# Optimization experiments

Measured on AMD Instinct MI355X. Metric: run time of the kernel, lower is better.

## Reference

```python
import jax, jax.numpy as jnp
import numpy as np

N = 8192          # num nodes
D = 512           # num_hidden
P = 512           # num_proj_hidden
TAU = 0.5
EPS = 1e-12       # F.normalize eps


def setup_inputs() -> dict:
    key = jax.random.key(0)
    k1, k2, k3, k4, k5, k6 = jax.random.split(key, 6)
    s1 = 1.0 / np.sqrt(D)  # torch Linear init bound
    s2 = 1.0 / np.sqrt(P)
    return {
        "z1": jax.random.normal(k1, (N, D), jnp.float32),
        "z2": jax.random.normal(k2, (N, D), jnp.float32),
        "index": jnp.arange(N, dtype=jnp.int32),  # all-unique -> unique() identity path
        "fc1_w": jax.random.uniform(k3, (D, P), jnp.float32, -s1, s1),
        "fc1_b": jax.random.uniform(k4, (P,), jnp.float32, -s1, s1),
        "fc2_w": jax.random.uniform(k5, (P, D), jnp.float32, -s2, s2),
        "fc2_b": jax.random.uniform(k6, (D,), jnp.float32, -s2, s2),
    }


def _projection(z, fc1_w, fc1_b, fc2_w, fc2_b):
    h = jax.nn.elu(z @ fc1_w + fc1_b)
    return h @ fc2_w + fc2_b


def _normalize(x):
    n = jnp.linalg.norm(x, axis=1, keepdims=True)
    return x / jnp.maximum(n, EPS)


def _semi_loss(a, b):
    an = _normalize(a)
    bn = _normalize(b)
    refl = jnp.exp((an @ an.T) / TAU)      # [N, N]
    btw = jnp.exp((an @ bn.T) / TAU)       # [N, N]
    denom = refl.sum(axis=1) + btw.sum(axis=1) - jnp.diagonal(refl)
    return -jnp.log(jnp.diagonal(btw) / denom)  # [N]


def reference(z1, z2, index, fc1_w, fc1_b, fc2_w, fc2_b):
    h1 = _projection(z1, fc1_w, fc1_b, fc2_w, fc2_b)
    h2 = _projection(z2, fc1_w, fc1_b, fc2_w, fc2_b)
    # index is all-unique (arange) -> unique() returns (h1, h2) unchanged
    l1 = _semi_loss(h1, h2)
    l2 = _semi_loss(h2, h1)
    return ((l1 + l2) * 0.5).mean()
```

## Files before the change

### kernel.cpp

```cpp
#include <hip/hip_runtime.h>
#include <hip/hip_bf16.h>

typedef __attribute__((ext_vector_type(8))) short short8;
typedef __attribute__((ext_vector_type(4))) short short4v;
typedef __attribute__((ext_vector_type(4))) float floatx4;
typedef __attribute__((ext_vector_type(2))) long longx2;
typedef __attribute__((ext_vector_type(2))) unsigned int uintx2;

#define NND 8192
#define DHID 512
#define TAU_INV 2.0f
#define CEXP 2.885390081777927f
#define E2 7.389056098930650f

__device__ inline unsigned short f2bf(float f) {
    union { float f; unsigned u; } v; v.f = f;
    unsigned r = v.u + 0x7FFFu + ((v.u >> 16) & 1u);
    return (unsigned short)(r >> 16);
}
__device__ inline float bf2f(short s) {
    union { unsigned u; float f; } v; v.u = ((unsigned)(unsigned short)s) << 16;
    return v.f;
}
__device__ inline float fp8dec(unsigned b) {
    b &= 0xFF;
    const unsigned s = b >> 7, e = (b >> 3) & 15, m = b & 7;
    float v;
    if (e == 0) v = (float)m * 0.001953125f;
    else { union { unsigned u; float f; } t; t.u = ((e + 120u) << 23) | (m << 20); v = t.f; }
    return s ? -v : v;
}

__device__ inline void gload_lds16(const void* g, void* l) {
    __builtin_amdgcn_global_load_lds(
        (const __attribute__((address_space(1))) unsigned int*)g,
        (__attribute__((address_space(3))) unsigned int*)l,
        16, 0, 0);
}

__global__ void cast_bf16_2(const float* __restrict__ z1, const float* __restrict__ z2,
                            short* __restrict__ out) {
    int i = blockIdx.x * 256 + threadIdx.x;
    const float* src = (i < 524288) ? z1 : z2;
    const int j = i & 524287;
    floatx4 v0 = ((const floatx4*)src)[2 * j];
    floatx4 v1 = ((const floatx4*)src)[2 * j + 1];
    short8 o;
    o[0] = (short)f2bf(v0[0]); o[1] = (short)f2bf(v0[1]);
    o[2] = (short)f2bf(v0[2]); o[3] = (short)f2bf(v0[3]);
    o[4] = (short)f2bf(v1[0]); o[5] = (short)f2bf(v1[1]);
    o[6] = (short)f2bf(v1[2]); o[7] = (short)f2bf(v1[3]);
    ((short8*)out)[i] = o;
}

__global__ void transpose_cast2(const float* __restrict__ a, const float* __restrict__ b,
                                short* __restrict__ oa, short* __restrict__ ob) {
    int idx = blockIdx.x * 256 + threadIdx.x;
    const float* in = (idx < 262144) ? a : b;
    short* out = (idx < 262144) ? oa : ob;
    idx &= 262143;
    int n = idx >> 9, k = idx & 511;
    out[(n << 9) + k] = (short)f2bf(in[(k << 9) + n]);
}

#define BK 32

template<int MODE>
__global__ __launch_bounds__(256, 2)
void gemm_nt(const short* __restrict__ A, const short* __restrict__ B, int N,
             const float* __restrict__ bias, short* __restrict__ outBf)
{
    __shared__ short As[128 * BK];
    __shared__ short Bs[128 * BK];

    const int tid  = threadIdx.x;
    const int m0 = blockIdx.x * 128;
    const int n0 = blockIdx.y * 128;
    const int wave = tid >> 6;
    const int lane = tid & 63;
    const int wr   = wave >> 1;
    const int wc   = wave & 1;
    const int lrow = lane & 15;
    const int lk   = lane >> 4;
    const int swq  = (lk ^ ((lrow >> 1) & 3)) * 8;

    floatx4 acc[4][4];
    floatx4 zero4 = {0.f, 0.f, 0.f, 0.f};
#pragma unroll
    for (int m = 0; m < 4; ++m)
#pragma unroll
        for (int n = 0; n < 4; ++n) acc[m][n] = zero4;

    for (int kt = 0; kt < 512 / BK; ++kt) {
        const int k0 = kt * BK;
        __syncthreads();
#pragma unroll
        for (int i = 0; i < 2; ++i) {
            const int chunk = i * 256 + tid;
            const int r = chunk >> 2;
            const int qq = chunk & 3;
            const int q = qq ^ ((r >> 1) & 3);
            gload_lds16(A + (size_t)(m0 + r) * 512 + k0 + q * 8, &As[r * 32 + qq * 8]);
            gload_lds16(B + (size_t)(n0 + r) * 512 + k0 + q * 8, &Bs[r * 32 + qq * 8]);
        }
        __syncthreads();
        short8 fa[4], fb[4];
#pragma unroll
        for (int m = 0; m < 4; ++m)
            fa[m] = *(const short8*)(&As[(wr * 64 + m * 16 + lrow) * 32 + swq]);
#pragma unroll
        for (int n = 0; n < 4; ++n)
            fb[n] = *(const short8*)(&Bs[(wc * 64 + n * 16 + lrow) * 32 + swq]);
#pragma unroll
        for (int m = 0; m < 4; ++m)
#pragma unroll
            for (int n = 0; n < 4; ++n)
                acc[m][n] = __builtin_amdgcn_mfma_f32_16x16x32_bf16(fa[m], fb[n], acc[m][n], 0, 0, 0);
    }

#pragma unroll
    for (int m = 0; m < 4; ++m) {
#pragma unroll
        for (int n = 0; n < 4; ++n) {
            const int gj = n0 + wc * 64 + n * 16 + lrow;
            const float bj = bias[gj];
#pragma unroll
            for (int r = 0; r < 4; ++r) {
                const int gi = m0 + wr * 64 + m * 16 + lk * 4 + r;
                float v = acc[m][n][r] + bj;
                if (MODE == 0) v = v > 0.f ? v : expm1f(v);
                outBf[(size_t)gi * N + gj] = (short)f2bf(v);
            }
        }
    }
}


__global__ __launch_bounds__(256, 3)
void gemm_gram(const unsigned char* __restrict__ Q, float* __restrict__ gpart)
{
    __shared__ unsigned char As[3][128 * 64];
    __shared__ unsigned char Bs[3][128 * 64];

    const int tid = threadIdx.x;
    const int wg = blockIdx.x;
    int bj = (int)((sqrtf(8.0f * (float)wg + 1.0f) - 1.0f) * 0.5f);
    if (bj < 0) bj = 0;
    if (bj > 127) bj = 127;
    while (bj > 0 && bj * (bj + 1) / 2 > wg) --bj;
    while ((bj + 1) * (bj + 2) / 2 <= wg) ++bj;
    const int bi = wg - bj * (bj + 1) / 2;
    const int m0 = bi * 128, n0 = bj * 128;

    const int wave = tid >> 6;
    const int lane = tid & 63;
    const int wr   = wave >> 1;
    const int wc   = wave & 1;
    const int lrow = lane & 15;
    const int lk   = lane >> 4;

    const int sr = tid >> 2;
    const int qL = tid & 3;
    const int qG = qL ^ ((sr >> 1) & 3);

#define STAGE_G(buf, k0) do { \
    gload_lds16(Q + (size_t)(m0 + sr) * 512 + (k0) + qG * 16,      &As[buf][ sr       * 64 + qL * 16]); \
    gload_lds16(Q + (size_t)(m0 + 64 + sr) * 512 + (k0) + qG * 16, &As[buf][(sr + 64) * 64 + qL * 16]); \
    gload_lds16(Q + (size_t)(n0 + sr) * 512 + (k0) + qG * 16,      &Bs[buf][ sr       * 64 + qL * 16]); \
    gload_lds16(Q + (size_t)(n0 + 64 + sr) * 512 + (k0) + qG * 16, &Bs[buf][(sr + 64) * 64 + qL * 16]); \
} while (0)

    floatx4 acc[4][4];
    floatx4 zero4 = {0.f, 0.f, 0.f, 0.f};
#pragma unroll
    for (int m = 0; m < 4; ++m)
#pragma unroll
        for (int n = 0; n < 4; ++n) acc[m][n] = zero4;

    STAGE_G(0, 0);
    STAGE_G(1, 64);
    asm volatile("s_waitcnt vmcnt(4)" ::: "memory");
    __builtin_amdgcn_s_barrier();

#pragma unroll
    for (int kt = 0; kt < 8; ++kt) {
        const int cur = kt % 3;
        if (kt + 2 < 8) STAGE_G((kt + 2) % 3, (kt + 2) * 64);
        longx2 fb[4];
#pragma unroll
        for (int n = 0; n < 4; ++n) {
            const int row = wc * 64 + n * 16 + lrow;
            fb[n] = *(const longx2*)&Bs[cur][(row << 6) + ((lk ^ ((row >> 1) & 3)) << 4)];
        }
#pragma unroll
        for (int m = 0; m < 4; ++m) {
            const int row = wr * 64 + m * 16 + lrow;
            const longx2 fa = *(const longx2*)&As[cur][(row << 6) + ((lk ^ ((row >> 1) & 3)) << 4)];
#pragma unroll
            for (int n = 0; n < 4; ++n) {
                acc[m][n] = __builtin_amdgcn_mfma_f32_16x16x32_fp8_fp8(fa[0], fb[n][0], acc[m][n], 0, 0, 0);
                acc[m][n] = __builtin_amdgcn_mfma_f32_16x16x32_fp8_fp8(fa[1], fb[n][1], acc[m][n], 0, 0, 0);
            }
        }
        if (kt < 6) asm volatile("s_waitcnt vmcnt(4)" ::: "memory");
        else        asm volatile("s_waitcnt vmcnt(0)" ::: "memory");
        __builtin_amdgcn_s_barrier();
    }
#undef STAGE_G

    float* lred = (float*)&As[0][0];

    float colpart[4] = {0.f, 0.f, 0.f, 0.f};
#pragma unroll
    for (int m = 0; m < 4; ++m) {
        float rowpart[4] = {0.f, 0.f, 0.f, 0.f};
#pragma unroll
        for (int n = 0; n < 4; ++n) {
#pragma unroll
            for (int r = 0; r < 4; ++r) {
                float v = exp2f(acc[m][n][r] * CEXP);
                rowpart[r] += v;
                colpart[n] += v;
            }
        }
#pragma unroll
        for (int r = 0; r < 4; ++r) {
            float t = rowpart[r];
            t += __shfl_xor(t, 1);
            t += __shfl_xor(t, 2);
            t += __shfl_xor(t, 4);
            t += __shfl_xor(t, 8);
            if (lrow == 0) lred[wc * 128 + wr * 64 + m * 16 + lk * 4 + r] = t;
        }
    }
#pragma unroll
    for (int n = 0; n < 4; ++n) {
        float t = colpart[n];
        t += __shfl_xor(t, 16);
        t += __shfl_xor(t, 32);
        if (lk == 0) lred[256 + wr * 128 + wc * 64 + n * 16 + lrow] = t;
    }
    __syncthreads();

    if (tid < 128) {
        gpart[(size_t)bj * (2 * NND) + m0 + tid] = lred[tid] + lred[128 + tid];
    } else if (m0 != n0) {
        const int c = tid - 128;
        gpart[(size_t)bi * (2 * NND) + n0 + c] = lred[256 + c] + lred[384 + c];
    }
}

__global__ void reduce_partials(const float* __restrict__ gpart, float* __restrict__ rsG) {
    const int i = blockIdx.x * 256 + threadIdx.x;
    float s = 0.f;
#pragma unroll 8
    for (int sl = 0; sl < 128; ++sl)
        s += gpart[(size_t)sl * (2 * NND) + i];
    rsG[i] = s;
}

__global__ void normalize_rows(const short* __restrict__ o, unsigned char* __restrict__ anq) {
    const int row = blockIdx.x;
    const int t = threadIdx.x;
    short4v v4 = ((const short4v*)(o + ((size_t)row << 9)))[t];
    const float a0 = bf2f(v4[0]), a1 = bf2f(v4[1]), a2 = bf2f(v4[2]), a3 = bf2f(v4[3]);
    float ss = a0 * a0 + a1 * a1 + a2 * a2 + a3 * a3;
    for (int m = 1; m < 64; m <<= 1) ss += __shfl_xor(ss, m);
    __shared__ float part[2];
    if ((t & 63) == 0) part[t >> 6] = ss;
    __syncthreads();
    const float sc = 1.f / fmaxf(sqrtf(part[0] + part[1]), 1e-12f);
    int w = __builtin_amdgcn_cvt_pk_fp8_f32(a0 * sc, a1 * sc, 0, false);
    w = __builtin_amdgcn_cvt_pk_fp8_f32(a2 * sc, a3 * sc, w, true);
    const int k = t * 4;
    const int b = k >> 6, kk = k & 63;
    const int addr = (row << 9) + (b << 6) + (((kk & 31) >> 3) << 4) + ((kk >> 5) << 3) + (kk & 7);
    *(int*)(anq + addr) = w;
}

__global__ void diag_dot(const unsigned char* __restrict__ q, float* __restrict__ d) {
    const int row = blockIdx.x * 4 + (threadIdx.x >> 6);
    const int lane = threadIdx.x & 63;
    uintx2 x = *(const uintx2*)(q + ((size_t)row << 9) + lane * 8);
    uintx2 y = *(const uintx2*)(q + ((size_t)(row + NND) << 9) + lane * 8);
    float s = 0.f;
#pragma unroll
    for (int w = 0; w < 2; ++w)
#pragma unroll
        for (int j = 0; j < 4; ++j)
            s += fp8dec(x[w] >> (8 * j)) * fp8dec(y[w] >> (8 * j));
    for (int m = 1; m < 64; m <<= 1) s += __shfl_xor(s, m);
    if (lane == 0) d[row] = s;
}

__global__ void final_reduce(const float* __restrict__ rsG,
                             const float* __restrict__ d12, float* __restrict__ out) {
    float s = 0.f;
    for (int i = threadIdx.x; i < NND; i += 256) {
        const float den1 = rsG[i] - E2;
        const float den2 = rsG[i + NND] - E2;
        s += 0.5f * (logf(den1) + logf(den2)) - d12[i] * TAU_INV;
    }
    for (int m = 1; m < 64; m <<= 1) s += __shfl_xor(s, m);
    __shared__ float part[4];
    const int lane = threadIdx.x & 63, w = threadIdx.x >> 6;
    if (lane == 0) part[w] = s;
    __syncthreads();
    if (threadIdx.x == 0) out[0] = (part[0] + part[1] + part[2] + part[3]) / (float)NND;
}

extern "C" void kernel_launch(void* const* d_in, const int* in_sizes, int n_in,
                              void* d_out, int out_size, void* d_ws, size_t ws_size,
                              hipStream_t stream) {
    const float* z1 = (const float*)d_in[0];
    const float* z2 = (const float*)d_in[1];
    const float* w1 = (const float*)d_in[3];
    const float* b1 = (const float*)d_in[4];
    const float* w2 = (const float*)d_in[5];
    const float* b2 = (const float*)d_in[6];
    float* out = (float*)d_out;

    char* p = (char*)d_ws;
    const size_t MATB = (size_t)2 * NND * DHID * 2;
    short* zb  = (short*)p;  p += MATB;
    short* hb  = (short*)p;  p += MATB;
    short* obuf = (short*)p; p += MATB;
    unsigned char* anq = (unsigned char*)p; p += (size_t)2 * NND * DHID;
    float* gpart = (float*)p; p += (size_t)128 * 2 * NND * 4;
    short* w1t = (short*)p;  p += 512 * 512 * 2;
    short* w2t = (short*)p;  p += 512 * 512 * 2;
    float* rsG = (float*)p;  p += (size_t)2 * NND * 4;
    float* d12 = (float*)p;  p += NND * 4;
    if ((size_t)(p - (char*)d_ws) > ws_size) return;

    transpose_cast2<<<2048, 256, 0, stream>>>(w1, w2, w1t, w2t);
    cast_bf16_2<<<4096, 256, 0, stream>>>(z1, z2, zb);
    gemm_nt<0><<<dim3(128, 4), 256, 0, stream>>>(zb, w1t, 512, b1, hb);
    gemm_nt<1><<<dim3(128, 4), 256, 0, stream>>>(hb, w2t, 512, b2, obuf);
    normalize_rows<<<2 * NND, 128, 0, stream>>>(obuf, anq);
    diag_dot<<<NND / 4, 256, 0, stream>>>(anq, d12);

    gemm_gram<<<8256, 256, 0, stream>>>(anq, gpart);
    reduce_partials<<<64, 256, 0, stream>>>(gpart, rsG);

    final_reduce<<<1, 256, 0, stream>>>(rsG, d12, out);
}
```

Baseline: 203.1 us.

## Fuse input bf16 cast into first GEMM and merge normalize with diagonal dot

The first projection GEMM now reads fp32 z1/z2 directly, converts to bf16 in registers and stores to LDS, which removes the separate cast kernel and its intermediate buffer. The normalization kernel now handles a row of both views at once and computes the positive-pair dot product from the bf16 values before fp8 quantization, so the diag_dot kernel goes away. The cost is that the A-tile load becomes synchronous register loads instead of direct global-to-LDS transfers, which may expose load latency in the GEMM. The diagonal term also changes slightly numerically because it is now computed from higher-precision values.

```diff
diff --git a/kernel.cpp b/kernel.cpp
--- a/kernel.cpp
+++ b/kernel.cpp
@@ -22,14 +22,6 @@
     union { unsigned u; float f; } v; v.u = ((unsigned)(unsigned short)s) << 16;
     return v.f;
 }
-__device__ inline float fp8dec(unsigned b) {
-    b &= 0xFF;
-    const unsigned s = b >> 7, e = (b >> 3) & 15, m = b & 7;
-    float v;
-    if (e == 0) v = (float)m * 0.001953125f;
-    else { union { unsigned u; float f; } t; t.u = ((e + 120u) << 23) | (m << 20); v = t.f; }
-    return s ? -v : v;
-}
 
 __device__ inline void gload_lds16(const void* g, void* l) {
     __builtin_amdgcn_global_load_lds(
@@ -38,19 +30,13 @@
         16, 0, 0);
 }
 
-__global__ void cast_bf16_2(const float* __restrict__ z1, const float* __restrict__ z2,
-                            short* __restrict__ out) {
-    int i = blockIdx.x * 256 + threadIdx.x;
-    const float* src = (i < 524288) ? z1 : z2;
-    const int j = i & 524287;
-    floatx4 v0 = ((const floatx4*)src)[2 * j];
-    floatx4 v1 = ((const floatx4*)src)[2 * j + 1];
+__device__ inline short8 cvt8(floatx4 a, floatx4 b) {
     short8 o;
-    o[0] = (short)f2bf(v0[0]); o[1] = (short)f2bf(v0[1]);
-    o[2] = (short)f2bf(v0[2]); o[3] = (short)f2bf(v0[3]);
-    o[4] = (short)f2bf(v1[0]); o[5] = (short)f2bf(v1[1]);
-    o[6] = (short)f2bf(v1[2]); o[7] = (short)f2bf(v1[3]);
-    ((short8*)out)[i] = o;
+    o[0] = (short)f2bf(a[0]); o[1] = (short)f2bf(a[1]);
+    o[2] = (short)f2bf(a[2]); o[3] = (short)f2bf(a[3]);
+    o[4] = (short)f2bf(b[0]); o[5] = (short)f2bf(b[1]);
+    o[6] = (short)f2bf(b[2]); o[7] = (short)f2bf(b[3]);
+    return o;
 }
 
 __global__ void transpose_cast2(const float* __restrict__ a, const float* __restrict__ b,
@@ -67,7 +53,8 @@
 
 template<int MODE>
 __global__ __launch_bounds__(256, 2)
-void gemm_nt(const short* __restrict__ A, const short* __restrict__ B, int N,
+void gemm_nt(const float* __restrict__ Az1, const float* __restrict__ Az2,
+             const short* __restrict__ Abf, const short* __restrict__ B,
              const float* __restrict__ bias, short* __restrict__ outBf)
 {
     __shared__ short As[128 * BK];
@@ -84,6 +71,14 @@
     const int lk   = lane >> 4;
     const int swq  = (lk ^ ((lrow >> 1) & 3)) * 8;
 
+    const int r0 = tid >> 2;
+    const int qq = tid & 3;
+    const int q  = qq ^ ((r0 >> 1) & 3);
+
+    const float* Asrc = (MODE == 0)
+        ? ((m0 < NND) ? Az1 + (size_t)m0 * 512 : Az2 + (size_t)(m0 - NND) * 512)
+        : nullptr;
+
     floatx4 acc[4][4];
     floatx4 zero4 = {0.f, 0.f, 0.f, 0.f};
 #pragma unroll
@@ -93,15 +88,26 @@
 
     for (int kt = 0; kt < 512 / BK; ++kt) {
         const int k0 = kt * BK;
+        floatx4 a00, a01, a10, a11;
+        if (MODE == 0) {
+            const float* p0 = Asrc + (size_t)r0 * 512 + k0 + q * 8;
+            const float* p1 = Asrc + (size_t)(r0 + 64) * 512 + k0 + q * 8;
+            a00 = *(const floatx4*)p0;  a01 = *(const floatx4*)(p0 + 4);
+            a10 = *(const floatx4*)p1;  a11 = *(const floatx4*)(p1 + 4);
+        }
         __syncthreads();
-#pragma unroll
-        for (int i = 0; i < 2; ++i) {
-            const int chunk = i * 256 + tid;
-            const int r = chunk >> 2;
-            const int qq = chunk & 3;
-            const int q = qq ^ ((r >> 1) & 3);
-            gload_lds16(A + (size_t)(m0 + r) * 512 + k0 + q * 8, &As[r * 32 + qq * 8]);
-            gload_lds16(B + (size_t)(n0 + r) * 512 + k0 + q * 8, &Bs[r * 32 + qq * 8]);
+        if (MODE == 0) {
+            *(short8*)&As[r0 * 32 + qq * 8]        = cvt8(a00, a01);
+            *(short8*)&As[(r0 + 64) * 32 + qq * 8] = cvt8(a10, a11);
+            gload_lds16(B + (size_t)(n0 + r0) * 512 + k0 + q * 8,        &Bs[r0 * 32 + qq * 8]);
+            gload_lds16(B + (size_t)(n0 + 64 + r0) * 512 + k0 + q * 8,   &Bs[(r0 + 64) * 32 + qq * 8]);
+        } else {
+#pragma unroll
+            for (int i = 0; i < 2; ++i) {
+                const int r = i * 64 + r0;
+                gload_lds16(Abf + (size_t)(m0 + r) * 512 + k0 + q * 8, &As[r * 32 + qq * 8]);
+                gload_lds16(B   + (size_t)(n0 + r) * 512 + k0 + q * 8, &Bs[r * 32 + qq * 8]);
+            }
         }
         __syncthreads();
         short8 fa[4], fb[4];
@@ -129,12 +135,11 @@
                 const int gi = m0 + wr * 64 + m * 16 + lk * 4 + r;
                 float v = acc[m][n][r] + bj;
                 if (MODE == 0) v = v > 0.f ? v : expm1f(v);
-                outBf[(size_t)gi * N + gj] = (short)f2bf(v);
+                outBf[(size_t)gi * 512 + gj] = (short)f2bf(v);
             }
         }
     }
 }
-
 
 __global__ __launch_bounds__(256, 3)
 void gemm_gram(const unsigned char* __restrict__ Q, float* __restrict__ gpart)
@@ -259,38 +264,41 @@
     rsG[i] = s;
 }
 
-__global__ void normalize_rows(const short* __restrict__ o, unsigned char* __restrict__ anq) {
+__global__ void normalize_diag(const short* __restrict__ o, unsigned char* __restrict__ anq,
+                               float* __restrict__ d12) {
     const int row = blockIdx.x;
     const int t = threadIdx.x;
-    short4v v4 = ((const short4v*)(o + ((size_t)row << 9)))[t];
-    const float a0 = bf2f(v4[0]), a1 = bf2f(v4[1]), a2 = bf2f(v4[2]), a3 = bf2f(v4[3]);
-    float ss = a0 * a0 + a1 * a1 + a2 * a2 + a3 * a3;
-    for (int m = 1; m < 64; m <<= 1) ss += __shfl_xor(ss, m);
-    __shared__ float part[2];
-    if ((t & 63) == 0) part[t >> 6] = ss;
+    short4v va = ((const short4v*)(o + ((size_t)row << 9)))[t];
+    short4v vb = ((const short4v*)(o + ((size_t)(row + NND) << 9)))[t];
+    const float a0 = bf2f(va[0]), a1 = bf2f(va[1]), a2 = bf2f(va[2]), a3 = bf2f(va[3]);
+    const float b0 = bf2f(vb[0]), b1 = bf2f(vb[1]), b2 = bf2f(vb[2]), b3 = bf2f(vb[3]);
+    float ssa = a0 * a0 + a1 * a1 + a2 * a2 + a3 * a3;
+    float ssb = b0 * b0 + b1 * b1 + b2 * b2 + b3 * b3;
+    float sd  = a0 * b0 + a1 * b1 + a2 * b2 + a3 * b3;
+    for (int m = 1; m < 64; m <<= 1) {
+        ssa += __shfl_xor(ssa, m);
+        ssb += __shfl_xor(ssb, m);
+        sd  += __shfl_xor(sd, m);
+    }
+    __shared__ float part[6];
+    if ((t & 63) == 0) {
+        const int w = (t >> 6) * 3;
+        part[w] = ssa; part[w + 1] = ssb; part[w + 2] = sd;
+    }
     __syncthreads();
-    const float sc = 1.f / fmaxf(sqrtf(part[0] + part[1]), 1e-12f);
-    int w = __builtin_amdgcn_cvt_pk_fp8_f32(a0 * sc, a1 * sc, 0, false);
-    w = __builtin_amdgcn_cvt_pk_fp8_f32(a2 * sc, a3 * sc, w, true);
+    const float sca = 1.f / fmaxf(sqrtf(part[0] + part[3]), 1e-12f);
+    const float scb = 1.f / fmaxf(sqrtf(part[1] + part[4]), 1e-12f);
+    if (t == 0) d12[row] = (part[2] + part[5]) * sca * scb;
+
     const int k = t * 4;
-    const int b = k >> 6, kk = k & 63;
-    const int addr = (row << 9) + (b << 6) + (((kk & 31) >> 3) << 4) + ((kk >> 5) << 3) + (kk & 7);
-    *(int*)(anq + addr) = w;
-}
-
-__global__ void diag_dot(const unsigned char* __restrict__ q, float* __restrict__ d) {
-    const int row = blockIdx.x * 4 + (threadIdx.x >> 6);
-    const int lane = threadIdx.x & 63;
-    uintx2 x = *(const uintx2*)(q + ((size_t)row << 9) + lane * 8);
-    uintx2 y = *(const uintx2*)(q + ((size_t)(row + NND) << 9) + lane * 8);
-    float s = 0.f;
-#pragma unroll
-    for (int w = 0; w < 2; ++w)
-#pragma unroll
-        for (int j = 0; j < 4; ++j)
-            s += fp8dec(x[w] >> (8 * j)) * fp8dec(y[w] >> (8 * j));
-    for (int m = 1; m < 64; m <<= 1) s += __shfl_xor(s, m);
-    if (lane == 0) d[row] = s;
+    const int bb = k >> 6, kk = k & 63;
+    const int off = (bb << 6) + (((kk & 31) >> 3) << 4) + ((kk >> 5) << 3) + (kk & 7);
+    int wa = __builtin_amdgcn_cvt_pk_fp8_f32(a0 * sca, a1 * sca, 0, false);
+    wa = __builtin_amdgcn_cvt_pk_fp8_f32(a2 * sca, a3 * sca, wa, true);
+    *(int*)(anq + (row << 9) + off) = wa;
+    int wb = __builtin_amdgcn_cvt_pk_fp8_f32(b0 * scb, b1 * scb, 0, false);
+    wb = __builtin_amdgcn_cvt_pk_fp8_f32(b2 * scb, b3 * scb, wb, true);
+    *(int*)(anq + ((size_t)(row + NND) << 9) + off) = wb;
 }
 
 __global__ void final_reduce(const float* __restrict__ rsG,
@@ -322,7 +330,6 @@
 
     char* p = (char*)d_ws;
     const size_t MATB = (size_t)2 * NND * DHID * 2;
-    short* zb  = (short*)p;  p += MATB;
     short* hb  = (short*)p;  p += MATB;
     short* obuf = (short*)p; p += MATB;
     unsigned char* anq = (unsigned char*)p; p += (size_t)2 * NND * DHID;
@@ -334,11 +341,9 @@
     if ((size_t)(p - (char*)d_ws) > ws_size) return;
 
     transpose_cast2<<<2048, 256, 0, stream>>>(w1, w2, w1t, w2t);
-    cast_bf16_2<<<4096, 256, 0, stream>>>(z1, z2, zb);
-    gemm_nt<0><<<dim3(128, 4), 256, 0, stream>>>(zb, w1t, 512, b1, hb);
-    gemm_nt<1><<<dim3(128, 4), 256, 0, stream>>>(hb, w2t, 512, b2, obuf);
-    normalize_rows<<<2 * NND, 128, 0, stream>>>(obuf, anq);
-    diag_dot<<<NND / 4, 256, 0, stream>>>(anq, d12);
+    gemm_nt<0><<<dim3(128, 4), 256, 0, stream>>>(z1, z2, nullptr, w1t, b1, hb);
+    gemm_nt<1><<<dim3(128, 4), 256, 0, stream>>>(nullptr, nullptr, hb, w2t, b2, obuf);
+    normalize_diag<<<NND, 128, 0, stream>>>(obuf, anq, d12);
 
     gemm_gram<<<8256, 256, 0, stream>>>(anq, gpart);
     reduce_partials<<<64, 256, 0, stream>>>(gpart, rsG);
```

Result: faster. 195.0 us (-4.0%).
